# Optimization experiments

Hardware: AMD Instinct MI355X
Metric: run time of the kernel (lower is better)

## Reference

```python
import jax, jax.numpy as jnp
import numpy as np

B, N_DET, N_T, NY, NX = 4, 128, 2048, 256, 256


def setup_inputs() -> dict:
    key = jax.random.key(0)
    k1, k2, k3 = jax.random.split(key, 3)
    sino = jax.random.normal(k1, (B, 1, N_DET, N_T), dtype=jnp.float32)
    # LUT channel 0: floor temporal index (stored as float, cast to int in forward)
    k_floor = jax.random.randint(k2, (NY, NX, N_DET), 0, N_T).astype(jnp.float32)
    # LUT channel 1: linear interpolation weight alpha in [0,1)
    alpha = jax.random.uniform(k3, (NY, NX, N_DET), dtype=jnp.float32)
    lut = jnp.stack([k_floor, alpha], axis=-1)  # [NY, NX, N_DET, 2]
    return {"sino": sino, "lut": lut}


def reference(sino, lut):
    # sino: [B, 1, n_det, n_t]; lut: [ny, nx, n_det, 2]
    b, c, n_det, n_t = sino.shape
    k_floor = lut[..., 0].astype(jnp.int32)          # [ny, nx, n_det]
    alpha = lut[..., 1]                               # [ny, nx, n_det]
    valid = (k_floor >= 0) & (k_floor < n_t - 1)
    k0 = jnp.clip(k_floor, 0, n_t - 2)
    k1 = k0 + 1
    S = sino[:, 0]                                    # [B, n_det, n_t]
    det = jnp.arange(n_det)                           # broadcasts against [ny,nx,n_det]
    s0 = S[:, det, k0]                                # [B, ny, nx, n_det]
    s1 = S[:, det, k1]                                # [B, ny, nx, n_det]
    sk = (1.0 - alpha) * s0 + alpha * s1
    sk = jnp.where(valid, sk, jnp.zeros_like(sk))
    # Hann apodization window over detectors
    apod = (0.5 - 0.5 * jnp.cos(2.0 * jnp.pi * jnp.arange(n_det, dtype=jnp.float32)
                                / max(n_det - 1, 1))).astype(sino.dtype)
    out = jnp.einsum('bijd,d->bij', sk, apod)
    norm = jnp.maximum(apod.sum(), 1e-06)
    out = out / norm
    return out[:, None]                               # [B, 1, ny, nx]
```

## Files before the change

kernel.cpp:

```cpp
#include <hip/hip_runtime.h>
#include <hip/hip_fp16.h>


#define NB      4
#define NDET    128
#define NT      2048
#define NPIX    65536
#define DBLOCK  8
#define NPHASE  2
#define PTILE   1024
#define THREADS 512
#define PXPT    (PTILE / THREADS)

__global__ __launch_bounds__(THREADS, 4)
void bp_kernel(const float* __restrict__ sino,
               const float* __restrict__ lut,
               float* __restrict__ out) {
    __shared__ __half2 lds[DBLOCK][NT];

    const int tid   = threadIdx.x;
    const int octet = blockIdx.x & 15;
    const int tile  = blockIdx.x >> 4;
    const int d0    = octet * DBLOCK;
    const int px0   = tile * PTILE;

    float apod[DBLOCK];
#pragma unroll
    for (int j = 0; j < DBLOCK; ++j) {
        float x = (float)(d0 + j) * (6.28318530717958647692f / 127.0f);
        apod[j] = 0.5f - 0.5f * __cosf(x);
    }

    float4 L[PXPT][4];
#pragma unroll
    for (int i = 0; i < PXPT; ++i) {
        const float4* lp = (const float4*)
            (lut + ((size_t)(px0 + tid + i * THREADS) * NDET + d0) * 2);
#pragma unroll
        for (int q = 0; q < 4; ++q) L[i][q] = lp[q];
    }

    float acc[PXPT][NB];
#pragma unroll
    for (int i = 0; i < PXPT; ++i)
#pragma unroll
        for (int b = 0; b < NB; ++b) acc[i][b] = 0.0f;

    for (int ph = 0; ph < NPHASE; ++ph) {
        const int b0 = ph * 2;
        if (ph) __syncthreads();

        for (int f = tid; f < DBLOCK * (NT / 4); f += THREADS) {
            int dl = f >> 9;
            int t4 = f & 511;
            const float4* s4 = (const float4*)sino;
            float4 ve = s4[((size_t)(b0 + 0) * NDET + (d0 + dl)) * (NT / 4) + t4];
            float4 vo = s4[((size_t)(b0 + 1) * NDET + (d0 + dl)) * (NT / 4) + t4];
            __half2* dst = &lds[dl][t4 * 4];
            dst[0] = __floats2half2_rn(ve.x, vo.x);
            dst[1] = __floats2half2_rn(ve.y, vo.y);
            dst[2] = __floats2half2_rn(ve.z, vo.z);
            dst[3] = __floats2half2_rn(ve.w, vo.w);
        }
        __syncthreads();

#pragma unroll
        for (int i = 0; i < PXPT; ++i) {
#pragma unroll
            for (int q = 0; q < 4; ++q) {
                float4 Lq = L[i][q];
#pragma unroll
                for (int h = 0; h < 2; ++h) {
                    float kf = h ? Lq.z : Lq.x;
                    float af = h ? Lq.w : Lq.y;
                    int   dl = q * 2 + h;

                    int k = (int)kf;
                    unsigned uk = (unsigned)k;
                    bool valid = uk < (unsigned)(NT - 1);
                    float w  = valid ? apod[dl] : 0.0f;
                    int  k0  = valid ? k : 0;
                    __half2 s0 = lds[dl][k0];
                    __half2 s1 = lds[dl][k0 + 1];
                    __half2 a2 = __float2half2_rn(af);
                    __half2 sk = __hfma2(a2, __hsub2(s1, s0), s0);
                    float2  fv = __half22float2(sk);
                    acc[i][b0 + 0] = fmaf(w, fv.x, acc[i][b0 + 0]);
                    acc[i][b0 + 1] = fmaf(w, fv.y, acc[i][b0 + 1]);
                }
            }
        }
    }

    const float inv_norm = 1.0f / 63.5f;
#pragma unroll
    for (int i = 0; i < PXPT; ++i) {
        const int px = px0 + tid + i * THREADS;
#pragma unroll
        for (int b = 0; b < NB; ++b) {
            atomicAdd(&out[(size_t)b * NPIX + px], acc[i][b] * inv_norm);
        }
    }
}

extern "C" void kernel_launch(void* const* d_in, const int* in_sizes, int n_in,
                              void* d_out, int out_size, void* d_ws, size_t ws_size,
                              hipStream_t stream) {
    const float* sino = (const float*)d_in[0];
    const float* lut  = (const float*)d_in[1];
    float* out = (float*)d_out;

    hipMemsetAsync(d_out, 0, (size_t)out_size * sizeof(float), stream);

    bp_kernel<<<dim3(1024), dim3(THREADS), 0, stream>>>(sino, lut, out);
}
```

Before: 129.7 us.

## Double-buffer sinogram staging in LDS and overlap global loads with gathers

The kernel now processes four phases of four detectors by two batches each, using a double-buffered LDS array of the same total size. Global sinogram loads for the next phase are issued into registers before the barrier, so their latency overlaps the LDS gather of the current phase. Atomic output writes for each finished batch pair are emitted early, and the LUT is read with nontemporal loads. In exchange, the staged loads hold extra vector registers, which may lower occupancy.

```diff
diff --git a/kernel.cpp b/kernel.cpp
--- a/kernel.cpp
+++ b/kernel.cpp
@@ -7,16 +7,18 @@
 #define NT      2048
 #define NPIX    65536
 #define DBLOCK  8
-#define NPHASE  2
+#define DPH     4
 #define PTILE   1024
 #define THREADS 512
 #define PXPT    (PTILE / THREADS)
+
+typedef float floatx4 __attribute__((ext_vector_type(4)));
 
 __global__ __launch_bounds__(THREADS, 4)
 void bp_kernel(const float* __restrict__ sino,
                const float* __restrict__ lut,
                float* __restrict__ out) {
-    __shared__ __half2 lds[DBLOCK][NT];
+    __shared__ __half2 lds[2][DPH][NT];
 
     const int tid   = threadIdx.x;
     const int octet = blockIdx.x & 15;
@@ -31,13 +33,13 @@
         apod[j] = 0.5f - 0.5f * __cosf(x);
     }
 
-    float4 L[PXPT][4];
+    floatx4 L[PXPT][4];
 #pragma unroll
     for (int i = 0; i < PXPT; ++i) {
-        const float4* lp = (const float4*)
+        const floatx4* lp = (const floatx4*)
             (lut + ((size_t)(px0 + tid + i * THREADS) * NDET + d0) * 2);
 #pragma unroll
-        for (int q = 0; q < 4; ++q) L[i][q] = lp[q];
+        for (int q = 0; q < 4; ++q) L[i][q] = __builtin_nontemporal_load(lp + q);
     }
 
     float acc[PXPT][NB];
@@ -46,61 +48,91 @@
 #pragma unroll
         for (int b = 0; b < NB; ++b) acc[i][b] = 0.0f;
 
-    for (int ph = 0; ph < NPHASE; ++ph) {
-        const int b0 = ph * 2;
-        if (ph) __syncthreads();
+    const floatx4* s4 = (const floatx4*)sino;
+    floatx4 ve[DPH], vo[DPH];
 
-        for (int f = tid; f < DBLOCK * (NT / 4); f += THREADS) {
-            int dl = f >> 9;
-            int t4 = f & 511;
-            const float4* s4 = (const float4*)sino;
-            float4 ve = s4[((size_t)(b0 + 0) * NDET + (d0 + dl)) * (NT / 4) + t4];
-            float4 vo = s4[((size_t)(b0 + 1) * NDET + (d0 + dl)) * (NT / 4) + t4];
-            __half2* dst = &lds[dl][t4 * 4];
-            dst[0] = __floats2half2_rn(ve.x, vo.x);
-            dst[1] = __floats2half2_rn(ve.y, vo.y);
-            dst[2] = __floats2half2_rn(ve.z, vo.z);
-            dst[3] = __floats2half2_rn(ve.w, vo.w);
+    auto stage_issue = [&](int p) {
+        const int b0  = (p >> 1) * 2;
+        const int dg0 = d0 + (p & 1) * DPH;
+#pragma unroll
+        for (int dl = 0; dl < DPH; ++dl) {
+            size_t row = ((size_t)b0 * NDET + dg0 + dl) * (NT / 4) + tid;
+            ve[dl] = s4[row];
+            vo[dl] = s4[row + (size_t)NDET * (NT / 4)];
         }
-        __syncthreads();
-
+    };
+    auto stage_write = [&](int p) {
+        const int buf = p & 1;
+#pragma unroll
+        for (int dl = 0; dl < DPH; ++dl) {
+            __half2* dst = &lds[buf][dl][tid * 4];
+            dst[0] = __floats2half2_rn(ve[dl].x, vo[dl].x);
+            dst[1] = __floats2half2_rn(ve[dl].y, vo[dl].y);
+            dst[2] = __floats2half2_rn(ve[dl].z, vo[dl].z);
+            dst[3] = __floats2half2_rn(ve[dl].w, vo[dl].w);
+        }
+    };
+    auto gather = [&](int p) {
+        const int b0  = (p >> 1) * 2;
+        const int dh  = p & 1;
+        const int buf = p & 1;
 #pragma unroll
         for (int i = 0; i < PXPT; ++i) {
 #pragma unroll
-            for (int q = 0; q < 4; ++q) {
-                float4 Lq = L[i][q];
+            for (int q2 = 0; q2 < 2; ++q2) {
+                floatx4 Lq = L[i][dh * 2 + q2];
 #pragma unroll
                 for (int h = 0; h < 2; ++h) {
                     float kf = h ? Lq.z : Lq.x;
                     float af = h ? Lq.w : Lq.y;
-                    int   dl = q * 2 + h;
-
+                    int   dl = q2 * 2 + h;
+                    int   j  = dh * DPH + dl;
                     int k = (int)kf;
-                    unsigned uk = (unsigned)k;
-                    bool valid = uk < (unsigned)(NT - 1);
-                    float w  = valid ? apod[dl] : 0.0f;
+                    bool valid = (unsigned)k < (unsigned)(NT - 1);
+                    float w  = valid ? apod[j] : 0.0f;
                     int  k0  = valid ? k : 0;
-                    __half2 s0 = lds[dl][k0];
-                    __half2 s1 = lds[dl][k0 + 1];
-                    __half2 a2 = __float2half2_rn(af);
-                    __half2 sk = __hfma2(a2, __hsub2(s1, s0), s0);
-                    float2  fv = __half22float2(sk);
+                    __half2 s0v = lds[buf][dl][k0];
+                    __half2 s1v = lds[buf][dl][k0 + 1];
+                    __half2 a2  = __float2half2_rn(af);
+                    __half2 sk  = __hfma2(a2, __hsub2(s1v, s0v), s0v);
+                    float2  fv  = __half22float2(sk);
                     acc[i][b0 + 0] = fmaf(w, fv.x, acc[i][b0 + 0]);
                     acc[i][b0 + 1] = fmaf(w, fv.y, acc[i][b0 + 1]);
                 }
             }
         }
-    }
-
+    };
     const float inv_norm = 1.0f / 63.5f;
+    auto emit = [&](int b) {
 #pragma unroll
-    for (int i = 0; i < PXPT; ++i) {
-        const int px = px0 + tid + i * THREADS;
-#pragma unroll
-        for (int b = 0; b < NB; ++b) {
+        for (int i = 0; i < PXPT; ++i) {
+            const int px = px0 + tid + i * THREADS;
             atomicAdd(&out[(size_t)b * NPIX + px], acc[i][b] * inv_norm);
         }
-    }
+    };
+
+    stage_issue(0);
+    stage_write(0);
+    stage_issue(1);
+    __syncthreads();
+
+    gather(0);
+    stage_write(1);
+    stage_issue(2);
+    __syncthreads();
+
+    gather(1);
+    emit(0); emit(1);
+    stage_write(2);
+    stage_issue(3);
+    __syncthreads();
+
+    gather(2);
+    stage_write(3);
+    __syncthreads();
+
+    gather(3);
+    emit(2); emit(3);
 }
 
 extern "C" void kernel_launch(void* const* d_in, const int* in_sizes, int n_in,
@@ -110,7 +142,7 @@
     const float* lut  = (const float*)d_in[1];
     float* out = (float*)d_out;
 
-    hipMemsetAsync(d_out, 0, (size_t)out_size * sizeof(float), stream);
+    (void)hipMemsetAsync(d_out, 0, (size_t)out_size * sizeof(float), stream);
 
     bp_kernel<<<dim3(1024), dim3(THREADS), 0, stream>>>(sino, lut, out);
 }
```

Result: slower. 161.4 us (+24.4%).

## Pack all four batches per sample in LDS and stage two detectors per phase

Applied to the files above, without the earlier changes.

The shared-memory layout changes so each time sample holds all four batches as two half2 values. Each phase now stages two detectors instead of eight detectors for half the batches. One interpolation then reads a contiguous 16-byte run covering s0 and s1 for every batch, replacing separate per-batch gathers. Halving LDS use allows a higher occupancy hint. The cost is four sync phases instead of two. The apodization weights are also made wave-uniform via readfirstlane.

```diff
diff --git a/kernel.cpp b/kernel.cpp
--- a/kernel.cpp
+++ b/kernel.cpp
@@ -7,16 +7,17 @@
 #define NT      2048
 #define NPIX    65536
 #define DBLOCK  8
-#define NPHASE  2
+#define DPH     2
+#define NPHASE  4
 #define PTILE   1024
 #define THREADS 512
 #define PXPT    (PTILE / THREADS)
 
-__global__ __launch_bounds__(THREADS, 4)
+__global__ __launch_bounds__(THREADS, 8)
 void bp_kernel(const float* __restrict__ sino,
                const float* __restrict__ lut,
                float* __restrict__ out) {
-    __shared__ __half2 lds[DBLOCK][NT];
+    __shared__ __half2 lds[DPH][NT][2];
 
     const int tid   = threadIdx.x;
     const int octet = blockIdx.x & 15;
@@ -28,16 +29,17 @@
 #pragma unroll
     for (int j = 0; j < DBLOCK; ++j) {
         float x = (float)(d0 + j) * (6.28318530717958647692f / 127.0f);
-        apod[j] = 0.5f - 0.5f * __cosf(x);
+        float v = 0.5f - 0.5f * __cosf(x);
+        apod[j] = __int_as_float(__builtin_amdgcn_readfirstlane(__float_as_int(v)));
     }
 
-    float4 L[PXPT][4];
+    float4 L[PXPT][NPHASE];
 #pragma unroll
     for (int i = 0; i < PXPT; ++i) {
         const float4* lp = (const float4*)
             (lut + ((size_t)(px0 + tid + i * THREADS) * NDET + d0) * 2);
 #pragma unroll
-        for (int q = 0; q < 4; ++q) L[i][q] = lp[q];
+        for (int q = 0; q < NPHASE; ++q) L[i][q] = lp[q];
     }
 
     float acc[PXPT][NB];
@@ -46,48 +48,55 @@
 #pragma unroll
         for (int b = 0; b < NB; ++b) acc[i][b] = 0.0f;
 
+    const float4* s4 = (const float4*)sino;
+
     for (int ph = 0; ph < NPHASE; ++ph) {
-        const int b0 = ph * 2;
+        const int dg0 = d0 + ph * DPH;
         if (ph) __syncthreads();
 
-        for (int f = tid; f < DBLOCK * (NT / 4); f += THREADS) {
+        for (int f = tid; f < DPH * (NT / 4); f += THREADS) {
             int dl = f >> 9;
             int t4 = f & 511;
-            const float4* s4 = (const float4*)sino;
-            float4 ve = s4[((size_t)(b0 + 0) * NDET + (d0 + dl)) * (NT / 4) + t4];
-            float4 vo = s4[((size_t)(b0 + 1) * NDET + (d0 + dl)) * (NT / 4) + t4];
-            __half2* dst = &lds[dl][t4 * 4];
-            dst[0] = __floats2half2_rn(ve.x, vo.x);
-            dst[1] = __floats2half2_rn(ve.y, vo.y);
-            dst[2] = __floats2half2_rn(ve.z, vo.z);
-            dst[3] = __floats2half2_rn(ve.w, vo.w);
+            size_t base = ((size_t)dg0 + dl) * (NT / 4) + t4;
+            float4 v0 = s4[base];
+            float4 v1 = s4[base + (size_t)1 * NDET * (NT / 4)];
+            float4 v2 = s4[base + (size_t)2 * NDET * (NT / 4)];
+            float4 v3 = s4[base + (size_t)3 * NDET * (NT / 4)];
+            __half2* dst = &lds[dl][t4 * 4][0];
+            dst[0] = __floats2half2_rn(v0.x, v1.x);
+            dst[1] = __floats2half2_rn(v2.x, v3.x);
+            dst[2] = __floats2half2_rn(v0.y, v1.y);
+            dst[3] = __floats2half2_rn(v2.y, v3.y);
+            dst[4] = __floats2half2_rn(v0.z, v1.z);
+            dst[5] = __floats2half2_rn(v2.z, v3.z);
+            dst[6] = __floats2half2_rn(v0.w, v1.w);
+            dst[7] = __floats2half2_rn(v2.w, v3.w);
         }
         __syncthreads();
 
 #pragma unroll
         for (int i = 0; i < PXPT; ++i) {
+            float4 Lq = L[i][ph];
 #pragma unroll
-            for (int q = 0; q < 4; ++q) {
-                float4 Lq = L[i][q];
-#pragma unroll
-                for (int h = 0; h < 2; ++h) {
-                    float kf = h ? Lq.z : Lq.x;
-                    float af = h ? Lq.w : Lq.y;
-                    int   dl = q * 2 + h;
-
-                    int k = (int)kf;
-                    unsigned uk = (unsigned)k;
-                    bool valid = uk < (unsigned)(NT - 1);
-                    float w  = valid ? apod[dl] : 0.0f;
-                    int  k0  = valid ? k : 0;
-                    __half2 s0 = lds[dl][k0];
-                    __half2 s1 = lds[dl][k0 + 1];
-                    __half2 a2 = __float2half2_rn(af);
-                    __half2 sk = __hfma2(a2, __hsub2(s1, s0), s0);
-                    float2  fv = __half22float2(sk);
-                    acc[i][b0 + 0] = fmaf(w, fv.x, acc[i][b0 + 0]);
-                    acc[i][b0 + 1] = fmaf(w, fv.y, acc[i][b0 + 1]);
-                }
+            for (int h = 0; h < 2; ++h) {
+                float kf = h ? Lq.z : Lq.x;
+                float af = h ? Lq.w : Lq.y;
+                int k = (int)kf;
+                bool valid = (unsigned)k < (unsigned)(NT - 1);
+                float w  = valid ? apod[ph * DPH + h] : 0.0f;
+                int  k0  = valid ? k : 0;
+                const __half2* q = &lds[h][k0][0];
+                __half2 s0a = q[0], s0b = q[1];
+                __half2 s1a = q[2], s1b = q[3];
+                __half2 a2  = __float2half2_rn(af);
+                __half2 ska = __hfma2(a2, __hsub2(s1a, s0a), s0a);
+                __half2 skb = __hfma2(a2, __hsub2(s1b, s0b), s0b);
+                float2 fa = __half22float2(ska);
+                float2 fb = __half22float2(skb);
+                acc[i][0] = fmaf(w, fa.x, acc[i][0]);
+                acc[i][1] = fmaf(w, fa.y, acc[i][1]);
+                acc[i][2] = fmaf(w, fb.x, acc[i][2]);
+                acc[i][3] = fmaf(w, fb.y, acc[i][3]);
             }
         }
     }
@@ -110,7 +119,7 @@
     const float* lut  = (const float*)d_in[1];
     float* out = (float*)d_out;
 
-    hipMemsetAsync(d_out, 0, (size_t)out_size * sizeof(float), stream);
+    (void)hipMemsetAsync(d_out, 0, (size_t)out_size * sizeof(float), stream);
 
     bp_kernel<<<dim3(1024), dim3(THREADS), 0, stream>>>(sino, lut, out);
 }
```

Result: slower. 175.7 us (+35.5%).

## Split detector block into two LDS phases to halve shared memory footprint

Applied to the files above, without the earlier changes.

Stages only four detectors of sinogram data in LDS per phase instead of eight, looping over four phases (batch pair × detector half). This halves the shared-memory allocation per block so more blocks can be resident per CU, improving latency hiding for the LDS gathers. In exchange it adds extra barriers and phase loop overhead with less work between syncs.

```diff
diff --git a/kernel.cpp b/kernel.cpp
--- a/kernel.cpp
+++ b/kernel.cpp
@@ -7,7 +7,8 @@
 #define NT      2048
 #define NPIX    65536
 #define DBLOCK  8
-#define NPHASE  2
+#define DPH     4
+#define NPHASE  4
 #define PTILE   1024
 #define THREADS 512
 #define PXPT    (PTILE / THREADS)
@@ -16,7 +17,7 @@
 void bp_kernel(const float* __restrict__ sino,
                const float* __restrict__ lut,
                float* __restrict__ out) {
-    __shared__ __half2 lds[DBLOCK][NT];
+    __shared__ __half2 lds[DPH][NT];
 
     const int tid   = threadIdx.x;
     const int octet = blockIdx.x & 15;
@@ -46,16 +47,21 @@
 #pragma unroll
         for (int b = 0; b < NB; ++b) acc[i][b] = 0.0f;
 
+    const float4* s4 = (const float4*)sino;
+
     for (int ph = 0; ph < NPHASE; ++ph) {
-        const int b0 = ph * 2;
+        const int bp  = ph >> 1;
+        const int dh  = ph & 1;
+        const int b0  = bp * 2;
+        const int dg0 = d0 + dh * DPH;
         if (ph) __syncthreads();
 
-        for (int f = tid; f < DBLOCK * (NT / 4); f += THREADS) {
+        for (int f = tid; f < DPH * (NT / 4); f += THREADS) {
             int dl = f >> 9;
             int t4 = f & 511;
-            const float4* s4 = (const float4*)sino;
-            float4 ve = s4[((size_t)(b0 + 0) * NDET + (d0 + dl)) * (NT / 4) + t4];
-            float4 vo = s4[((size_t)(b0 + 1) * NDET + (d0 + dl)) * (NT / 4) + t4];
+            size_t row = ((size_t)b0 * NDET + dg0 + dl) * (NT / 4) + t4;
+            float4 ve = s4[row];
+            float4 vo = s4[row + (size_t)NDET * (NT / 4)];
             __half2* dst = &lds[dl][t4 * 4];
             dst[0] = __floats2half2_rn(ve.x, vo.x);
             dst[1] = __floats2half2_rn(ve.y, vo.y);
@@ -67,24 +73,22 @@
 #pragma unroll
         for (int i = 0; i < PXPT; ++i) {
 #pragma unroll
-            for (int q = 0; q < 4; ++q) {
-                float4 Lq = L[i][q];
+            for (int q2 = 0; q2 < 2; ++q2) {
+                float4 Lq = L[i][dh * 2 + q2];
 #pragma unroll
                 for (int h = 0; h < 2; ++h) {
                     float kf = h ? Lq.z : Lq.x;
                     float af = h ? Lq.w : Lq.y;
-                    int   dl = q * 2 + h;
-
+                    int   dl = q2 * 2 + h;
                     int k = (int)kf;
-                    unsigned uk = (unsigned)k;
-                    bool valid = uk < (unsigned)(NT - 1);
-                    float w  = valid ? apod[dl] : 0.0f;
+                    bool valid = (unsigned)k < (unsigned)(NT - 1);
+                    float w  = valid ? apod[dh * DPH + dl] : 0.0f;
                     int  k0  = valid ? k : 0;
-                    __half2 s0 = lds[dl][k0];
-                    __half2 s1 = lds[dl][k0 + 1];
-                    __half2 a2 = __float2half2_rn(af);
-                    __half2 sk = __hfma2(a2, __hsub2(s1, s0), s0);
-                    float2  fv = __half22float2(sk);
+                    __half2 s0v = lds[dl][k0];
+                    __half2 s1v = lds[dl][k0 + 1];
+                    __half2 a2  = __float2half2_rn(af);
+                    __half2 sk  = __hfma2(a2, __hsub2(s1v, s0v), s0v);
+                    float2  fv  = __half22float2(sk);
                     acc[i][b0 + 0] = fmaf(w, fv.x, acc[i][b0 + 0]);
                     acc[i][b0 + 1] = fmaf(w, fv.y, acc[i][b0 + 1]);
                 }
@@ -110,7 +114,7 @@
     const float* lut  = (const float*)d_in[1];
     float* out = (float*)d_out;
 
-    hipMemsetAsync(d_out, 0, (size_t)out_size * sizeof(float), stream);
+    (void)hipMemsetAsync(d_out, 0, (size_t)out_size * sizeof(float), stream);
 
     bp_kernel<<<dim3(1024), dim3(THREADS), 0, stream>>>(sino, lut, out);
 }
```

Result: faster. 127.1 us (-2.0%).
